# Kernel optimization log

Measured on AMD Instinct MI355X. Metric: run time of the kernel, lower is better.

Reference implementation:

```python
import jax, jax.numpy as jnp
import numpy as np

T, B, D = 2048, 16, 1024


def setup_inputs() -> dict:
    key = jax.random.key(0)
    ks = jax.random.split(key, 4)
    x = jax.random.normal(ks[0], (T, B, D), dtype=jnp.float32)
    z = jax.random.normal(ks[1], (T, B, D), dtype=jnp.float32)
    h0 = jnp.zeros((B, D), dtype=jnp.float32)
    # xavier-uniform-ish W_x, scaled near-orthogonal-ish W_h (random normal scaled)
    W_x = jax.random.normal(ks[2], (D, D), dtype=jnp.float32) * (1.0 / np.sqrt(D))
    W_h = jax.random.normal(ks[3], (D, D), dtype=jnp.float32) * (0.9 / np.sqrt(D))
    b = jnp.zeros((D,), dtype=jnp.float32)
    g_z = jnp.ones((D,), dtype=jnp.float32)
    g_h = jnp.zeros((D,), dtype=jnp.float32)
    b_gate = jnp.zeros((D,), dtype=jnp.float32)
    return {"x": x, "z": z, "h0": h0, "W_x": W_x, "W_h": W_h, "b": b,
            "g_z": g_z, "g_h": g_h, "b_gate": b_gate}


def reference(x, z, h0, W_x, W_h, b, g_z, g_h, b_gate):
    # Precompute the input projection for all timesteps in one big GEMM.
    xp = jnp.einsum('tbd,ed->tbe', x, W_x) + b  # [T,B,D]

    def step(h_prev, inp):
        xp_t, z_t = inp
        h_new = jnp.tanh(xp_t + h_prev @ W_h.T)           # [B,D]
        gate = jax.nn.silu(z_t * g_z + h_new * g_h + b_gate)
        out = h_new * gate
        return h_new, (out, h_new)

    _, (output, hs) = jax.lax.scan(step, h0, (xp, z))
    h = jnp.concatenate([h0[None], hs], axis=0)  # [T+1,B,D]
    return output, h
```

## Files before the change

kernel.cpp:

```cpp
#include <hip/hip_runtime.h>
#include <stdint.h>

#define T_STEPS 2048
#define BATCH   16
#define DIM     1024

typedef float  f32x4  __attribute__((ext_vector_type(4)));
typedef __bf16 bf16x8 __attribute__((ext_vector_type(8)));

__global__ void prep_kernel(const float* __restrict__ h0,
                            float* __restrict__ hout,
                            unsigned long long* __restrict__ hX) {
  int i = blockIdx.x * blockDim.x + threadIdx.x;
  if (i < BATCH * DIM) {
    float v = h0[i];
    hout[i] = v;
    hX[i] = (unsigned long long)__float_as_uint(v);
    hX[BATCH * DIM + i] = 0xFFFFFFFF00000000ull;
  }
}

__global__ __launch_bounds__(256)
void xp_gemm(const float* __restrict__ X, const float* __restrict__ W,
             const float* __restrict__ Bv, float* __restrict__ XP) {
  __shared__ __bf16 As[128 * 64];
  __shared__ __bf16 Bs[128 * 64];
  const int tid = threadIdx.x;
  const int bm = blockIdx.x & 255;
  const int bn = blockIdx.x >> 8;
  const int w = tid >> 6, l = tid & 63;
  const int wr = w >> 1, wc = w & 1;
  const int sr = tid >> 1, sh = tid & 1;

  const float* xrow = X + (size_t)(bm * 128 + sr) * DIM + sh * 32;
  const float* wrow = W + (size_t)(bn * 128 + sr) * DIM + sh * 32;
  char* AsB = (char*)As;
  char* BsB = (char*)Bs;
  const int swr  = sr * 128;
  const int swzs = (sr & 7) << 4;

  f32x4 acc[4][4];
  const f32x4 z4 = {0.f, 0.f, 0.f, 0.f};
#pragma unroll
  for (int i = 0; i < 4; ++i)
#pragma unroll
    for (int j = 0; j < 4; ++j) acc[i][j] = z4;

  for (int kt = 0; kt < 16; ++kt) {
#pragma unroll
    for (int j = 0; j < 8; ++j) {
      f32x4 a  = *(const f32x4*)(xrow + kt * 64 + 4 * j);
      f32x4 bv = *(const f32x4*)(wrow + kt * 64 + 4 * j);
      union { __bf16 h[4]; unsigned long long u; } pa, pb;
#pragma unroll
      for (int q = 0; q < 4; ++q) { pa.h[q] = (__bf16)a[q]; pb.h[q] = (__bf16)bv[q]; }
      int c2  = (sh * 32 + 4 * j) * 2;
      int off = swr + (c2 ^ swzs);
      *(unsigned long long*)(AsB + off) = pa.u;
      *(unsigned long long*)(BsB + off) = pb.u;
    }
    __syncthreads();
#pragma unroll
    for (int ks = 0; ks < 2; ++ks) {
      bf16x8 afr[4], bfr[4];
#pragma unroll
      for (int mi = 0; mi < 4; ++mi) {
        int row = wr * 64 + mi * 16 + (l & 15);
        int c2  = ks * 64 + (l >> 4) * 16;
        afr[mi] = *(const bf16x8*)(AsB + row * 128 + (c2 ^ ((row & 7) << 4)));
      }
#pragma unroll
      for (int ni = 0; ni < 4; ++ni) {
        int row = wc * 64 + ni * 16 + (l & 15);
        int c2  = ks * 64 + (l >> 4) * 16;
        bfr[ni] = *(const bf16x8*)(BsB + row * 128 + (c2 ^ ((row & 7) << 4)));
      }
#pragma unroll
      for (int mi = 0; mi < 4; ++mi)
#pragma unroll
        for (int ni = 0; ni < 4; ++ni)
          acc[mi][ni] = __builtin_amdgcn_mfma_f32_16x16x32_bf16(
              afr[mi], bfr[ni], acc[mi][ni], 0, 0, 0);
    }
    __syncthreads();
  }
  const int colb = bn * 128 + wc * 64 + (l & 15);
#pragma unroll
  for (int ni = 0; ni < 4; ++ni) {
    int col = colb + ni * 16;
    float bb = Bv[col];
#pragma unroll
    for (int mi = 0; mi < 4; ++mi) {
      int row = bm * 128 + wr * 64 + mi * 16 + ((l >> 4) << 2);
#pragma unroll
      for (int r = 0; r < 4; ++r)
        XP[(size_t)(row + r) * DIM + col] = acc[mi][ni][r] + bb;
    }
  }
}

__global__ __launch_bounds__(1024, 4)
void rnn_kernel(const float* __restrict__ Wh,
                const float* __restrict__ Z,
                const float* __restrict__ gz,
                const float* __restrict__ gh,
                const float* __restrict__ bg,
                float* __restrict__ out,
                float* __restrict__ hout,
                unsigned long long* __restrict__ hX) {
  __shared__ float hb[2][1024];
  const int b   = blockIdx.x >> 4;
  const int s   = blockIdx.x & 15;
  const int tid = threadIdx.x;
  const int w   = tid >> 6;
  const int l   = tid & 63;
  const int r0  = s * 64;
  const int myrow  = r0 + w * 4 + (l & 3);
  const bool writer = (l < 4);

  f32x4 W4[4][4];
  {
    const f32x4* WhV = (const f32x4*)Wh;
#pragma unroll
    for (int r4 = 0; r4 < 4; ++r4) {
      size_t base = (size_t)(r0 + w * 4 + r4) * (DIM / 4) + l * 4;
#pragma unroll
      for (int jj = 0; jj < 4; ++jj) W4[r4][jj] = WhV[base + jj];
    }
  }

  float cgz = 0.f, cgh = 0.f, cbg = 0.f, xp_n = 0.f, z_n = 0.f;
  if (writer) {
    cgz = gz[myrow]; cgh = gh[myrow]; cbg = bg[myrow];
    xp_n = out[(size_t)b * DIM + myrow];
    z_n  = Z[(size_t)b * DIM + myrow];
  }

  unsigned long long* hx0 = hX + (size_t)b * DIM;
  unsigned long long* hx1 = hX + (size_t)(BATCH + b) * DIM;
  const int swz_w = tid ^ (((tid >> 5) & 7) << 2);

  for (int t = 0; t < T_STEPS; ++t) {
    unsigned long long* src = (t & 1) ? hx1 : hx0;
    unsigned long long* dst = (t & 1) ? hx0 : hx1;
    unsigned long long v;
    int spins = 0;
    do {
      v = __hip_atomic_load(&src[tid], __ATOMIC_RELAXED, __HIP_MEMORY_SCOPE_AGENT);
    } while ((unsigned)(v >> 32) != (unsigned)t && ++spins < 4096);
    hb[t & 1][swz_w] = __uint_as_float((unsigned)v);
    __syncthreads();
    float acc0 = 0.f, acc1 = 0.f, acc2 = 0.f, acc3 = 0.f;
#pragma unroll
    for (int jj = 0; jj < 4; ++jj) {
      int word = ((l << 4) | (jj << 2)) ^ (((l >> 1) & 7) << 2);
      f32x4 h4 = *(const f32x4*)&hb[t & 1][word];
#pragma unroll
      for (int i = 0; i < 4; ++i) {
        acc0 = fmaf(W4[0][jj][i], h4[i], acc0);
        acc1 = fmaf(W4[1][jj][i], h4[i], acc1);
        acc2 = fmaf(W4[2][jj][i], h4[i], acc2);
        acc3 = fmaf(W4[3][jj][i], h4[i], acc3);
      }
    }
#pragma unroll
    for (int m = 32; m >= 1; m >>= 1) {
      acc0 += __shfl_xor(acc0, m);
      acc1 += __shfl_xor(acc1, m);
      acc2 += __shfl_xor(acc2, m);
      acc3 += __shfl_xor(acc3, m);
    }
    if (writer) {
      float accm = (l == 0) ? acc0 : (l == 1) ? acc1 : (l == 2) ? acc2 : acc3;
      float pre = accm + xp_n;
      float e2 = __expf(2.0f * pre);
      float hn = 1.0f - 2.0f / (e2 + 1.0f);
      unsigned long long pk = ((unsigned long long)(unsigned)(t + 1) << 32)
                            | (unsigned long long)__float_as_uint(hn);
      __hip_atomic_store(&dst[myrow], pk, __ATOMIC_RELAXED, __HIP_MEMORY_SCOPE_AGENT);
      hout[((size_t)(t + 1) * BATCH + b) * DIM + myrow] = hn;
      float y   = z_n * cgz + hn * cgh + cbg;
      float sig = 1.0f / (1.0f + __expf(-y));
      out[((size_t)t * BATCH + b) * DIM + myrow] = hn * (y * sig);
      if (t + 1 < T_STEPS) {
        xp_n = out[((size_t)(t + 1) * BATCH + b) * DIM + myrow];
        z_n  = Z[((size_t)(t + 1) * BATCH + b) * DIM + myrow];
      }
    }
  }
}

extern "C" void kernel_launch(void* const* d_in, const int* in_sizes, int n_in,
                              void* d_out, int out_size, void* d_ws, size_t ws_size,
                              hipStream_t stream) {
  const float* x    = (const float*)d_in[0];
  const float* z    = (const float*)d_in[1];
  const float* h0   = (const float*)d_in[2];
  const float* Wx   = (const float*)d_in[3];
  const float* Wh   = (const float*)d_in[4];
  const float* bias = (const float*)d_in[5];
  const float* gz   = (const float*)d_in[6];
  const float* gh   = (const float*)d_in[7];
  const float* bg   = (const float*)d_in[8];

  float* out  = (float*)d_out;
  float* hout = out + (size_t)T_STEPS * BATCH * DIM;
  unsigned long long* hX = (unsigned long long*)d_ws;

  prep_kernel<<<dim3(64), dim3(256), 0, stream>>>(h0, hout, hX);
  xp_gemm<<<dim3(2048), dim3(256), 0, stream>>>(x, Wx, bias, out);
  rnn_kernel<<<dim3(256), dim3(1024), 0, stream>>>(Wh, z, gz, gh, bg, out, hout, hX);
}
```

Before: 6.484 ms.

## Poll hidden state with a single wave using wide loads and transpose-reduce rows

The per-step spin-wait moves from all 16 waves to a single wave. That wave polls the whole 1024-entry state vector with eight dwordx4 inline-asm loads (sc1), checks every tag, and sleeps briefly between polls before scattering the values into shared memory. This is meant to cut L2 polling traffic and contention from many waves on the critical path of each timestep. The 4-row butterfly reduction becomes a transpose-style reduce that needs 6 shuffles instead of 24. The trade-off is that the polling wave now serialises the wait, and the spin limit rises to 1<<22.

```diff
diff --git a/kernel.cpp b/kernel.cpp
--- a/kernel.cpp
+++ b/kernel.cpp
@@ -5,8 +5,10 @@
 #define BATCH   16
 #define DIM     1024
 
-typedef float  f32x4  __attribute__((ext_vector_type(4)));
-typedef __bf16 bf16x8 __attribute__((ext_vector_type(8)));
+typedef float    f32x4 __attribute__((ext_vector_type(4)));
+typedef float    f32x2 __attribute__((ext_vector_type(2)));
+typedef unsigned u32x4 __attribute__((ext_vector_type(4)));
+typedef __bf16   bf16x8 __attribute__((ext_vector_type(8)));
 
 __global__ void prep_kernel(const float* __restrict__ h0,
                             float* __restrict__ hout,
@@ -100,20 +102,18 @@
 }
 
 __global__ __launch_bounds__(1024, 4)
-void rnn_kernel(const float* __restrict__ Wh,
-                const float* __restrict__ Z,
-                const float* __restrict__ gz,
-                const float* __restrict__ gh,
+void rnn_kernel(const float* __restrict__ Wh, const float* __restrict__ Z,
+                const float* __restrict__ gz, const float* __restrict__ gh,
                 const float* __restrict__ bg,
                 float* __restrict__ out,
                 float* __restrict__ hout,
                 unsigned long long* __restrict__ hX) {
   __shared__ float hb[2][1024];
-  const int b   = blockIdx.x >> 4;
-  const int s   = blockIdx.x & 15;
   const int tid = threadIdx.x;
   const int w   = tid >> 6;
   const int l   = tid & 63;
+  const int b   = blockIdx.x >> 4;
+  const int s   = blockIdx.x & 15;
   const int r0  = s * 64;
   const int myrow  = r0 + w * 4 + (l & 3);
   const bool writer = (l < 4);
@@ -138,18 +138,49 @@
 
   unsigned long long* hx0 = hX + (size_t)b * DIM;
   unsigned long long* hx1 = hX + (size_t)(BATCH + b) * DIM;
-  const int swz_w = tid ^ (((tid >> 5) & 7) << 2);
 
   for (int t = 0; t < T_STEPS; ++t) {
     unsigned long long* src = (t & 1) ? hx1 : hx0;
     unsigned long long* dst = (t & 1) ? hx0 : hx1;
-    unsigned long long v;
-    int spins = 0;
-    do {
-      v = __hip_atomic_load(&src[tid], __ATOMIC_RELAXED, __HIP_MEMORY_SCOPE_AGENT);
-    } while ((unsigned)(v >> 32) != (unsigned)t && ++spins < 4096);
-    hb[t & 1][swz_w] = __uint_as_float((unsigned)v);
+
+    if (w == 0) {
+      const char* a0 = (const char*)src + 16 * l;
+      const char* a1 = a0 + 4096;
+      const unsigned tt = (unsigned)t;
+      u32x4 q0, q1, q2, q3, q4, q5, q6, q7;
+      int spins = 0;
+      for (;;) {
+        asm volatile(
+            "global_load_dwordx4 %[q0], %[a0], off sc1\n\t"
+            "global_load_dwordx4 %[q1], %[a0], off offset:1024 sc1\n\t"
+            "global_load_dwordx4 %[q2], %[a0], off offset:2048 sc1\n\t"
+            "global_load_dwordx4 %[q3], %[a0], off offset:3072 sc1\n\t"
+            "global_load_dwordx4 %[q4], %[a1], off sc1\n\t"
+            "global_load_dwordx4 %[q5], %[a1], off offset:1024 sc1\n\t"
+            "global_load_dwordx4 %[q6], %[a1], off offset:2048 sc1\n\t"
+            "global_load_dwordx4 %[q7], %[a1], off offset:3072 sc1\n\t"
+            "s_waitcnt vmcnt(0)"
+            : [q0]"=v"(q0), [q1]"=v"(q1), [q2]"=v"(q2), [q3]"=v"(q3),
+              [q4]"=v"(q4), [q5]"=v"(q5), [q6]"=v"(q6), [q7]"=v"(q7)
+            : [a0]"v"(a0), [a1]"v"(a1)
+            : "memory");
+        int ok = (q0.y == tt) & (q0.w == tt) & (q1.y == tt) & (q1.w == tt) &
+                 (q2.y == tt) & (q2.w == tt) & (q3.y == tt) & (q3.w == tt) &
+                 (q4.y == tt) & (q4.w == tt) & (q5.y == tt) & (q5.w == tt) &
+                 (q6.y == tt) & (q6.w == tt) & (q7.y == tt) & (q7.w == tt);
+        if (__all(ok)) break;
+        if (++spins >= (1 << 22)) break;
+        __builtin_amdgcn_s_sleep(2);
+      }
+#define SCAT(J, Q) { int w0 = 2 * l + 128 * J; w0 ^= ((w0 >> 5) & 7) << 2; \
+      f32x2 p; p.x = __uint_as_float(Q.x); p.y = __uint_as_float(Q.z);      \
+      *(f32x2*)&hb[t & 1][w0] = p; }
+      SCAT(0, q0) SCAT(1, q1) SCAT(2, q2) SCAT(3, q3)
+      SCAT(4, q4) SCAT(5, q5) SCAT(6, q6) SCAT(7, q7)
+#undef SCAT
+    }
     __syncthreads();
+
     float acc0 = 0.f, acc1 = 0.f, acc2 = 0.f, acc3 = 0.f;
 #pragma unroll
     for (int jj = 0; jj < 4; ++jj) {
@@ -163,16 +194,19 @@
         acc3 = fmaf(W4[3][jj][i], h4[i], acc3);
       }
     }
-#pragma unroll
-    for (int m = 32; m >= 1; m >>= 1) {
-      acc0 += __shfl_xor(acc0, m);
-      acc1 += __shfl_xor(acc1, m);
-      acc2 += __shfl_xor(acc2, m);
-      acc3 += __shfl_xor(acc3, m);
-    }
+    float w01 = (l & 1) ? acc0 : acc1;
+    float v01 = ((l & 1) ? acc1 : acc0) + __shfl_xor(w01, 1);
+    float w23 = (l & 1) ? acc2 : acc3;
+    float v23 = ((l & 1) ? acc3 : acc2) + __shfl_xor(w23, 1);
+    float wv  = (l & 2) ? v01 : v23;
+    float vv  = ((l & 2) ? v23 : v01) + __shfl_xor(wv, 2);
+    vv += __shfl_xor(vv, 4);
+    vv += __shfl_xor(vv, 8);
+    vv += __shfl_xor(vv, 16);
+    vv += __shfl_xor(vv, 32);
+
     if (writer) {
-      float accm = (l == 0) ? acc0 : (l == 1) ? acc1 : (l == 2) ? acc2 : acc3;
-      float pre = accm + xp_n;
+      float pre = vv + xp_n;
       float e2 = __expf(2.0f * pre);
       float hn = 1.0f - 2.0f / (e2 + 1.0f);
       unsigned long long pk = ((unsigned long long)(unsigned)(t + 1) << 32)
```

After: 5.547 ms. 1.17x faster.

## Pack hidden-state exchange as tagged bf16 quads polled by a single wave

Applied to the files above, without the earlier changes.

The cross-block hidden-state exchange now uses 16-byte slots. Each slot holds four bf16 values with a step tag at both ends, so one dwordx4 store/load with sc1 carries four elements and is validated by the tags. Only wave 0 polls the slots, retrying just the pending chunks, and scatters the expanded floats into shared memory. The step loop is unrolled by two with double-buffered xp/z prefetch, and the cross-lane reduction uses a transpose-style shuffle to cut shuffle count. This cuts exchange traffic and polling cost, at the price of quantizing the recurrent h input to bf16, which adds accuracy risk.

```diff
diff --git a/kernel.cpp b/kernel.cpp
--- a/kernel.cpp
+++ b/kernel.cpp
@@ -4,19 +4,33 @@
 #define T_STEPS 2048
 #define BATCH   16
 #define DIM     1024
-
-typedef float  f32x4  __attribute__((ext_vector_type(4)));
-typedef __bf16 bf16x8 __attribute__((ext_vector_type(8)));
+#define BD      (BATCH * DIM)
+#define SLOTS   4096
+
+typedef float    f32x4 __attribute__((ext_vector_type(4)));
+typedef unsigned u32x4 __attribute__((ext_vector_type(4)));
+typedef __bf16   bf16x8 __attribute__((ext_vector_type(8)));
+
+__device__ __forceinline__ unsigned bf16b(float f) {
+  __bf16 b = (__bf16)f; unsigned short s; __builtin_memcpy(&s, &b, 2);
+  return (unsigned)s;
+}
 
 __global__ void prep_kernel(const float* __restrict__ h0,
                             float* __restrict__ hout,
-                            unsigned long long* __restrict__ hX) {
+                            u32x4* __restrict__ hX4) {
   int i = blockIdx.x * blockDim.x + threadIdx.x;
-  if (i < BATCH * DIM) {
-    float v = h0[i];
-    hout[i] = v;
-    hX[i] = (unsigned long long)__float_as_uint(v);
-    hX[BATCH * DIM + i] = 0xFFFFFFFF00000000ull;
+  if (i < BD) hout[i] = h0[i];
+  if (i < SLOTS) {
+    int b = i >> 8, j = i & 255;
+    const float* hp = h0 + b * DIM + 4 * j;
+    u32x4 v;
+    v.x = 0u; v.w = 0u;
+    v.y = bf16b(hp[0]) | (bf16b(hp[1]) << 16);
+    v.z = bf16b(hp[2]) | (bf16b(hp[3]) << 16);
+    hX4[i] = v;
+    u32x4 inv; inv.x = 0xFFFFFFFFu; inv.w = 0xFFFFFFFFu; inv.y = 0u; inv.z = 0u;
+    hX4[SLOTS + i] = inv;
   }
 }
 
@@ -53,7 +67,7 @@
       f32x4 bv = *(const f32x4*)(wrow + kt * 64 + 4 * j);
       union { __bf16 h[4]; unsigned long long u; } pa, pb;
 #pragma unroll
-      for (int q = 0; q < 4; ++q) { pa.h[q] = (__bf16)a[q]; pb.h[q] = (__bf16)bv[q]; }
+      for (int qq = 0; qq < 4; ++qq) { pa.h[qq] = (__bf16)a[qq]; pb.h[qq] = (__bf16)bv[qq]; }
       int c2  = (sh * 32 + 4 * j) * 2;
       int off = swr + (c2 ^ swzs);
       *(unsigned long long*)(AsB + off) = pa.u;
@@ -99,21 +113,20 @@
   }
 }
 
-__global__ __launch_bounds__(1024, 4)
-void rnn_kernel(const float* __restrict__ Wh,
-                const float* __restrict__ Z,
-                const float* __restrict__ gz,
-                const float* __restrict__ gh,
+__global__ __attribute__((amdgpu_flat_work_group_size(1024, 1024)))
+__attribute__((amdgpu_waves_per_eu(4, 4)))
+void rnn_kernel(const float* __restrict__ Wh, const float* __restrict__ Z,
+                const float* __restrict__ gz, const float* __restrict__ gh,
                 const float* __restrict__ bg,
                 float* __restrict__ out,
                 float* __restrict__ hout,
-                unsigned long long* __restrict__ hX) {
+                u32x4* __restrict__ hX4) {
   __shared__ float hb[2][1024];
-  const int b   = blockIdx.x >> 4;
-  const int s   = blockIdx.x & 15;
   const int tid = threadIdx.x;
   const int w   = tid >> 6;
   const int l   = tid & 63;
+  const int b   = blockIdx.x >> 4;
+  const int s   = blockIdx.x & 15;
   const int r0  = s * 64;
   const int myrow  = r0 + w * 4 + (l & 3);
   const bool writer = (l < 4);
@@ -129,65 +142,107 @@
     }
   }
 
-  float cgz = 0.f, cgh = 0.f, cbg = 0.f, xp_n = 0.f, z_n = 0.f;
+  float cgz = 0.f, cgh = 0.f, cbg = 0.f;
+  float xpA = 0.f, zA = 0.f, xpB = 0.f, zB = 0.f;
   if (writer) {
     cgz = gz[myrow]; cgh = gh[myrow]; cbg = bg[myrow];
-    xp_n = out[(size_t)b * DIM + myrow];
-    z_n  = Z[(size_t)b * DIM + myrow];
-  }
-
-  unsigned long long* hx0 = hX + (size_t)b * DIM;
-  unsigned long long* hx1 = hX + (size_t)(BATCH + b) * DIM;
-  const int swz_w = tid ^ (((tid >> 5) & 7) << 2);
-
-  for (int t = 0; t < T_STEPS; ++t) {
-    unsigned long long* src = (t & 1) ? hx1 : hx0;
-    unsigned long long* dst = (t & 1) ? hx0 : hx1;
-    unsigned long long v;
-    int spins = 0;
-    do {
-      v = __hip_atomic_load(&src[tid], __ATOMIC_RELAXED, __HIP_MEMORY_SCOPE_AGENT);
-    } while ((unsigned)(v >> 32) != (unsigned)t && ++spins < 4096);
-    hb[t & 1][swz_w] = __uint_as_float((unsigned)v);
-    __syncthreads();
-    float acc0 = 0.f, acc1 = 0.f, acc2 = 0.f, acc3 = 0.f;
-#pragma unroll
-    for (int jj = 0; jj < 4; ++jj) {
-      int word = ((l << 4) | (jj << 2)) ^ (((l >> 1) & 7) << 2);
-      f32x4 h4 = *(const f32x4*)&hb[t & 1][word];
-#pragma unroll
-      for (int i = 0; i < 4; ++i) {
-        acc0 = fmaf(W4[0][jj][i], h4[i], acc0);
-        acc1 = fmaf(W4[1][jj][i], h4[i], acc1);
-        acc2 = fmaf(W4[2][jj][i], h4[i], acc2);
-        acc3 = fmaf(W4[3][jj][i], h4[i], acc3);
-      }
-    }
-#pragma unroll
-    for (int m = 32; m >= 1; m >>= 1) {
-      acc0 += __shfl_xor(acc0, m);
-      acc1 += __shfl_xor(acc1, m);
-      acc2 += __shfl_xor(acc2, m);
-      acc3 += __shfl_xor(acc3, m);
-    }
-    if (writer) {
-      float accm = (l == 0) ? acc0 : (l == 1) ? acc1 : (l == 2) ? acc2 : acc3;
-      float pre = accm + xp_n;
-      float e2 = __expf(2.0f * pre);
-      float hn = 1.0f - 2.0f / (e2 + 1.0f);
-      unsigned long long pk = ((unsigned long long)(unsigned)(t + 1) << 32)
-                            | (unsigned long long)__float_as_uint(hn);
-      __hip_atomic_store(&dst[myrow], pk, __ATOMIC_RELAXED, __HIP_MEMORY_SCOPE_AGENT);
-      hout[((size_t)(t + 1) * BATCH + b) * DIM + myrow] = hn;
-      float y   = z_n * cgz + hn * cgh + cbg;
-      float sig = 1.0f / (1.0f + __expf(-y));
-      out[((size_t)t * BATCH + b) * DIM + myrow] = hn * (y * sig);
-      if (t + 1 < T_STEPS) {
-        xp_n = out[((size_t)(t + 1) * BATCH + b) * DIM + myrow];
-        z_n  = Z[((size_t)(t + 1) * BATCH + b) * DIM + myrow];
-      }
-    }
-  }
+    xpA = out[(size_t)b * DIM + myrow];
+    zA  = Z[(size_t)b * DIM + myrow];
+  }
+
+#define TAGOK(Q) __all((int)((Q.x == tt) & (Q.w == tt)))
+#define SCAT(K, Q, P) { int qi = 64 * K + l; int wi = ((qi ^ (qi >> 3)) & 255) << 2; \
+    f32x4 v; v.x = __uint_as_float(Q.y << 16);                                       \
+    v.y = __uint_as_float(Q.y & 0xFFFF0000u);                                        \
+    v.z = __uint_as_float(Q.z << 16);                                                \
+    v.w = __uint_as_float(Q.z & 0xFFFF0000u);                                        \
+    *(f32x4*)&hb[P][wi] = v; }
+
+#define STEP(P, XPC, ZC, XPN, ZN)                                                  \
+  {                                                                                \
+    const unsigned tt = (unsigned)t;                                               \
+    const u32x4* srcq = hX4 + (size_t)(P) * SLOTS + (size_t)b * 256;               \
+    u32x4*       dstq = hX4 + (size_t)(P ^ 1) * SLOTS + (size_t)b * 256;           \
+    if (w == 0) {                                                                  \
+      const char* ap = (const char*)srcq + (l << 4);                               \
+      u32x4 q0, q1, q2, q3;                                                        \
+      unsigned pend = 0xFu; int rounds = 0;                                        \
+      do {                                                                         \
+        if (pend & 1u) asm volatile("global_load_dwordx4 %0, %1, off sc1"          \
+                                    : "=v"(q0) : "v"(ap) : "memory");              \
+        if (pend & 2u) asm volatile("global_load_dwordx4 %0, %1, off offset:1024 sc1" \
+                                    : "=v"(q1) : "v"(ap) : "memory");              \
+        if (pend & 4u) asm volatile("global_load_dwordx4 %0, %1, off offset:2048 sc1" \
+                                    : "=v"(q2) : "v"(ap) : "memory");              \
+        if (pend & 8u) asm volatile("global_load_dwordx4 %0, %1, off offset:3072 sc1" \
+                                    : "=v"(q3) : "v"(ap) : "memory");              \
+        asm volatile("s_waitcnt vmcnt(0)" ::: "memory");                           \
+        if ((pend & 1u) && TAGOK(q0)) { SCAT(0, q0, P); pend &= ~1u; }             \
+        if ((pend & 2u) && TAGOK(q1)) { SCAT(1, q1, P); pend &= ~2u; }             \
+        if ((pend & 4u) && TAGOK(q2)) { SCAT(2, q2, P); pend &= ~4u; }             \
+        if ((pend & 8u) && TAGOK(q3)) { SCAT(3, q3, P); pend &= ~8u; }             \
+      } while (pend && ++rounds < (1 << 22));                                      \
+    }                                                                              \
+            \
+    if (writer && t + 1 < T_STEPS) {                                               \
+      XPN = out[((size_t)(t + 1) * BATCH + b) * DIM + myrow];                      \
+      ZN  = Z[((size_t)(t + 1) * BATCH + b) * DIM + myrow];                        \
+    }                                                                              \
+    __syncthreads();                                                               \
+    float acc0 = 0.f, acc1 = 0.f, acc2 = 0.f, acc3 = 0.f;                          \
+    _Pragma("unroll")                                                              \
+    for (int jj = 0; jj < 4; ++jj) {                                               \
+      int qr = 4 * l + jj;                                                         \
+      int wb = ((qr ^ (qr >> 3)) & 255) << 2;                                      \
+      f32x4 h4 = *(const f32x4*)&hb[P][wb];                                        \
+      _Pragma("unroll")                                                            \
+      for (int i = 0; i < 4; ++i) {                                                \
+        acc0 = fmaf(W4[0][jj][i], h4[i], acc0);                                    \
+        acc1 = fmaf(W4[1][jj][i], h4[i], acc1);                                    \
+        acc2 = fmaf(W4[2][jj][i], h4[i], acc2);                                    \
+        acc3 = fmaf(W4[3][jj][i], h4[i], acc3);                                    \
+      }                                                                            \
+    }                                                                              \
+    float w01 = (l & 1) ? acc0 : acc1;                                             \
+    float v01 = ((l & 1) ? acc1 : acc0) + __shfl_xor(w01, 1);                      \
+    float w23 = (l & 1) ? acc2 : acc3;                                             \
+    float v23 = ((l & 1) ? acc3 : acc2) + __shfl_xor(w23, 1);                      \
+    float wv  = (l & 2) ? v01 : v23;                                               \
+    float vv  = ((l & 2) ? v23 : v01) + __shfl_xor(wv, 2);                         \
+    vv += __shfl_xor(vv, 4);                                                       \
+    vv += __shfl_xor(vv, 8);                                                       \
+    vv += __shfl_xor(vv, 16);                                                      \
+    vv += __shfl_xor(vv, 32);                                                      \
+    if (writer) {                                                                  \
+      float pre = vv + XPC;                                                        \
+      float e2 = __expf(2.0f * pre);                                               \
+      float hn = 1.0f - 2.0f / (e2 + 1.0f);                                        \
+      float h1 = __shfl(hn, 1), h2 = __shfl(hn, 2), h3 = __shfl(hn, 3);            \
+      if (l == 0) {                                                                \
+        u32x4 pk;                                                                  \
+        pk.x = tt + 1u; pk.w = tt + 1u;                                            \
+        pk.y = bf16b(hn) | (bf16b(h1) << 16);                                      \
+        pk.z = bf16b(h2) | (bf16b(h3) << 16);                                      \
+        u32x4* pp = dstq + (s * 16 + w);                                           \
+        asm volatile("global_store_dwordx4 %0, %1, off sc1"                        \
+                     :: "v"(pp), "v"(pk) : "memory");                              \
+      }                                                                            \
+      hout[((size_t)(t + 1) * BATCH + b) * DIM + myrow] = hn;                      \
+      float y   = ZC * cgz + hn * cgh + cbg;                                       \
+      float sig = 1.0f / (1.0f + __expf(-y));                                      \
+      out[((size_t)t * BATCH + b) * DIM + myrow] = hn * (y * sig);                 \
+    }                                                                              \
+  }
+
+  for (int t = 0; t < T_STEPS; ) {
+    STEP(0, xpA, zA, xpB, zB)
+    ++t;
+    STEP(1, xpB, zB, xpA, zA)
+    ++t;
+  }
+#undef STEP
+#undef SCAT
+#undef TAGOK
 }
 
 extern "C" void kernel_launch(void* const* d_in, const int* in_sizes, int n_in,
@@ -205,9 +260,9 @@
 
   float* out  = (float*)d_out;
   float* hout = out + (size_t)T_STEPS * BATCH * DIM;
-  unsigned long long* hX = (unsigned long long*)d_ws;
-
-  prep_kernel<<<dim3(64), dim3(256), 0, stream>>>(h0, hout, hX);
+  u32x4* hX4  = (u32x4*)d_ws;
+
+  prep_kernel<<<dim3(64), dim3(256), 0, stream>>>(h0, hout, hX4);
   xp_gemm<<<dim3(2048), dim3(256), 0, stream>>>(x, Wx, bias, out);
-  rnn_kernel<<<dim3(256), dim3(1024), 0, stream>>>(Wh, z, gz, gh, bg, out, hout, hX);
-}
+  rnn_kernel<<<dim3(256), dim3(1024), 0, stream>>>(Wh, z, gz, gh, bg, out, hout, hX4);
+}
```

Measured after the change: 6.667 ms. 1.03x slower.
